# Optimization experiments

Measured on AMD Instinct MI355X. Metric: run time of the kernel, lower is better.

## Reference

```python
import jax, jax.numpy as jnp
import numpy as np

# Static configuration matching init_kwargs
LR_SHAPES = ((64, 64), (128, 128), (256, 256))
H0, W0 = LR_SHAPES[0]          # selected layer (layer_number = 0)
UP = (8, 8)                     # upscale factors -> output_dim = 64
OUT_DIM = UP[0] * UP[1]
KERNEL = (3, 3)
PAD = (1, 1)
BATCH = 64
WEIGHTS_IN = 189                # 9 + 36 + 144


def _unfold(x, kernel, stride, pad):
    """torch.F.unfold equivalent for NCHW input with C==1.
    x: (N, 1, H, W) -> (N, kh*kw, L) with row-major spatial positions."""
    patches = jax.lax.conv_general_dilated_patches(
        x,
        filter_shape=kernel,
        window_strides=stride,
        padding=((pad[0], pad[0]), (pad[1], pad[1])),
        dimension_numbers=('NCHW', 'OIHW', 'NCHW'),
    )  # (N, kh*kw, H_out, W_out)
    n, k, h, w = patches.shape
    return patches.reshape(n, k, h * w)


def setup_inputs() -> dict:
    key = jax.random.key(0)
    k0, k1, k2, kw = jax.random.split(key, 4)
    x0 = jax.random.normal(k0, (BATCH, 1, 64, 64), dtype=jnp.float32)
    x1 = jax.random.normal(k1, (BATCH, 1, 128, 128), dtype=jnp.float32)
    x2 = jax.random.normal(k2, (BATCH, 1, 256, 256), dtype=jnp.float32)
    # original uses uniform(-stdv, stdv) with tiny stdv; small-scale normal keeps
    # the softmax non-degenerate while matching the magnitude regime
    weight = jax.random.normal(kw, (WEIGHTS_IN, OUT_DIM), dtype=jnp.float32) * 0.01
    return {"x0": x0, "x1": x1, "x2": x2, "weight": weight}


def reference(x0, x1, x2, weight):
    xs = (x0, x1, x2)
    cols = []
    for j, (hj, wj) in enumerate(LR_SHAPES):
        s = (hj // H0, wj // W0)                       # scale vs selected layer
        f = (KERNEL[0] * s[0], KERNEL[1] * s[1])       # scaled kernel
        p = (PAD[0] * s[0], PAD[1] * s[1])             # scaled padding
        cols.append(_unfold(xs[j], f, s, p))           # (N, 9*s0*s1, L)
    X = jnp.concatenate(cols, axis=1)                  # (N, 189, L), L = H0*W0

    # per-pixel attention weights: matmul + ReLU + softmax
    logits = jax.nn.relu(jnp.einsum('nkl,ko->nlo', X, weight))  # (N, L, 64)
    soft = jax.nn.softmax(logits, axis=-1)                       # (N, L, 64)

    # reassemble: each LR pixel value scaled by its 64 attention weights (C==1)
    xsel = x0.reshape(x0.shape[0], H0 * W0)            # (N, L)
    out = xsel[:, :, None] * soft                      # (N, L, 64)

    # fold(kernel=1) == reshape to (N, 64, H0, W0)
    n = out.shape[0]
    out = out.transpose(0, 2, 1).reshape(n, OUT_DIM, H0, W0)

    # pixel shuffle -> (N, 1, H0*up0, W0*up1)
    out = out.reshape(n, 1, UP[0], UP[1], H0, W0)
    out = out.transpose(0, 1, 4, 2, 5, 3)
    return out.reshape(n, 1, H0 * UP[0], W0 * UP[1])
```

## Files before the change

kernel.cpp:

```cpp
#include <hip/hip_runtime.h>

typedef _Float16 f16;
typedef f16 f16x8 __attribute__((ext_vector_type(8)));
typedef f16 f16x4 __attribute__((ext_vector_type(4)));
typedef float f32x4 __attribute__((ext_vector_type(4)));

#define X0OFF 0
#define X1OFF 140
#define X2OFF 524
#define WSL   2048
#define LOG2E 1.4426950408889634f

__global__ void prep_wt(const float* __restrict__ W, f16* __restrict__ Wt) {
  const int f = blockIdx.x * 256 + threadIdx.x;
  const int s = f >> 8;
  const int t = (f >> 6) & 3;
  const int lane = f & 63;
  const int quad = lane >> 4, ln = lane & 15;
  const int n = t * 16 + ln;
  f16 vals[8];
  #pragma unroll
  for (int j = 0; j < 8; ++j) {
    int kp = s * 32 + quad * 8 + j;
    int orig = -1;
    if (kp < 16)      { int ki = kp >> 2, kj = kp & 3;                   if (ki < 3 && kj < 3) orig = 3*ki + kj; }
    else if (kp < 64) { int kk = kp - 16; int ki = kk >> 3, kj = kk & 7;  if (kj < 6)          orig = 9 + 6*ki + kj; }
    else              { int kk = kp - 64; int ki = kk >> 4, kj = kk & 15; if (kj < 12)         orig = 45 + 12*ki + kj; }
    vals[j] = (f16)((orig >= 0) ? W[orig * 64 + n] : 0.f);
  }
  *(f16x8*)(Wt + (size_t)f * 8) = *(const f16x8*)vals;
}

__global__ __launch_bounds__(256, 6) void fuse_kernel(
    const float* __restrict__ x0, const float* __restrict__ x1,
    const float* __restrict__ x2, const f16* __restrict__ Wt,
    float* __restrict__ out)
{
  __shared__ __align__(16) f16 tiles[4 * WSL];

  const int tid  = threadIdx.x;
  const int bid  = ((blockIdx.x & 7) << 8) | (blockIdx.x >> 3);
  const int nb   = bid >> 5;
  const int ty8  = (bid >> 2) & 7;
  const int tx   = bid & 3;
  const int lane = tid & 63;
  const int wid  = tid >> 6;
  const int ln   = lane & 15;
  const int quad = lane >> 4;

  f16* sl = tiles + wid * WSL;
  const f16* __restrict__ wfrag = Wt + (size_t)lane * 8;

  f32x4 v2[6];
  {
    const float* img = x2 + nb * 65536;
    #pragma unroll
    for (int i = 0; i < 6; ++i) {
      int idx = lane + 64 * i;
      int rr = idx / 22, c4 = idx - rr * 22;
      int gy = ty8 * 32 - 4 + 8 * wid + rr;
      int gx = tx * 64 - 8 + 4 * c4;
      bool inb = (i < 5 || lane < 32) && ((unsigned)gy < 256u) && ((unsigned)gx < 256u);
      v2[i] = inb ? *(const f32x4*)(img + gy * 256 + gx) : (f32x4){0.f, 0.f, 0.f, 0.f};
    }
  }

  {
    const float* img = x1 + nb * 16384;
    #pragma unroll
    for (int i = 0; i < 2; ++i) {
      int idx = lane + 64 * i;
      int rr = idx / 11, c4 = idx - rr * 11;
      int gy = ty8 * 16 - 2 + 4 * wid + rr;
      int gx = tx * 32 - 4 + 4 * c4;
      bool ok  = (i < 1 || lane < 24);
      bool inb = ok && ((unsigned)gy < 128u) && ((unsigned)gx < 128u);
      f32x4 t = inb ? *(const f32x4*)(img + gy * 128 + gx) : (f32x4){0.f, 0.f, 0.f, 0.f};
      if (ok) {
        f16x4 h; h[0] = (f16)t[0]; h[1] = (f16)t[1]; h[2] = (f16)t[2]; h[3] = (f16)t[3];
        *(f16x4*)&sl[X1OFF + rr * 48 + 4 * c4] = h;
      }
    }
  }
  {
    const float* img = x0 + nb * 4096;
    int rr = lane / 6, c4 = lane - rr * 6;
    int gy = ty8 * 8 - 1 + 2 * wid + rr;
    int gx = tx * 16 - 4 + 4 * c4;
    bool ok  = lane < 30;
    bool inb = ok && ((unsigned)gy < 64u) && ((unsigned)gx < 64u);
    f32x4 t = inb ? *(const f32x4*)(img + gy * 64 + gx) : (f32x4){0.f, 0.f, 0.f, 0.f};
    if (ok) {
      f16x4 h; h[0] = (f16)t[0]; h[1] = (f16)t[1]; h[2] = (f16)t[2]; h[3] = (f16)t[3];
      *(f16x4*)&sl[X0OFF + rr * 28 + 4 * c4] = h;
    }
  }

  float xs[2];
  #pragma unroll
  for (int cc = 0; cc < 2; ++cc)
    xs[cc] = x0[nb * 4096 + (ty8 * 8 + 2 * wid + cc) * 64 + tx * 16 + ln];

  #pragma unroll
  for (int i = 0; i < 6; ++i) {
    if (i < 5 || lane < 32) {
      int idx = lane + 64 * i;
      int rr = idx / 22, c4 = idx - rr * 22;
      f16x4 h; h[0] = (f16)v2[i][0]; h[1] = (f16)v2[i][1];
      h[2] = (f16)v2[i][2]; h[3] = (f16)v2[i][3];
      *(f16x4*)&sl[X2OFF + rr * 92 + 4 * c4] = h;
    }
  }

  f16x8 bf0[4];
  #pragma unroll
  for (int t = 0; t < 4; ++t)
    bf0[t] = *(const f16x8*)(wfrag + t * 512);


  f32x4 acc[2][4];
  #pragma unroll
  for (int c = 0; c < 2; ++c)
    #pragma unroll
    for (int t = 0; t < 4; ++t)
      acc[c][t] = (f32x4){0.f, 0.f, 0.f, 0.f};

  {
    #pragma unroll
    for (int cc = 0; cc < 2; ++cc) {
      f16x8 a;
      if (quad < 2) {
        const int a0 = X0OFF + (cc + 2 * quad) * 28 + ln + 3;
        #pragma unroll
        for (int j = 0; j < 4; ++j) a[j]     = sl[a0 + j];
        #pragma unroll
        for (int j = 0; j < 4; ++j) a[4 + j] = sl[a0 + 28 + j];
      } else {
        const int a1 = X1OFF + (2 * cc + quad - 2) * 48 + 2 * ln + 2;
        #pragma unroll
        for (int j = 0; j < 8; ++j) a[j] = sl[a1 + j];
      }
      #pragma unroll
      for (int t = 0; t < 4; ++t)
        acc[cc][t] = __builtin_amdgcn_mfma_f32_16x16x32_f16(bf0[t], a, acc[cc][t], 0, 0, 0);
    }
  }
  {
    f16x8 bf[4];
    #pragma unroll
    for (int t = 0; t < 4; ++t)
      bf[t] = *(const f16x8*)(wfrag + (4 + t) * 512);
    #pragma unroll
    for (int cc = 0; cc < 2; ++cc) {
      const int a1 = X1OFF + (2 * cc + 2 + quad) * 48 + 2 * ln + 2;
      f16x8 a;
      #pragma unroll
      for (int j = 0; j < 8; ++j) a[j] = sl[a1 + j];
      #pragma unroll
      for (int t = 0; t < 4; ++t)
        acc[cc][t] = __builtin_amdgcn_mfma_f32_16x16x32_f16(bf[t], a, acc[cc][t], 0, 0, 0);
    }
  }
  #pragma unroll 3
  for (int s = 2; s < 8; ++s) {
    f16x8 bf[4];
    #pragma unroll
    for (int t = 0; t < 4; ++t)
      bf[t] = *(const f16x8*)(wfrag + (s * 4 + t) * 512);
    #pragma unroll
    for (int cc = 0; cc < 2; ++cc) {
      const int b2 = X2OFF + (4 * cc + 2 * (s - 2) + (quad >> 1)) * 92 + 4 * ln + 4 + 8 * (quad & 1);
      f16x4 lo = *(const f16x4*)&sl[b2];
      f16x4 hi = *(const f16x4*)&sl[b2 + 4];
      f16x8 a;
      a[0] = lo[0]; a[1] = lo[1]; a[2] = lo[2]; a[3] = lo[3];
      a[4] = hi[0]; a[5] = hi[1]; a[6] = hi[2]; a[7] = hi[3];
      #pragma unroll
      for (int t = 0; t < 4; ++t)
        acc[cc][t] = __builtin_amdgcn_mfma_f32_16x16x32_f16(bf[t], a, acc[cc][t], 0, 0, 0);
    }
  }

  const int gx8 = (tx * 16 + ln) * 8;
  #pragma unroll
  for (int cc = 0; cc < 2; ++cc) {
    float v[4][4];
    float m = 0.f;
    #pragma unroll
    for (int t = 0; t < 4; ++t)
      #pragma unroll
      for (int r = 0; r < 4; ++r) {
        float x = fmaxf(acc[cc][t][r], 0.f);
        v[t][r] = x;
        m = fmaxf(m, x);
      }
    m = fmaxf(m, __shfl_xor(m, 16));
    m = fmaxf(m, __shfl_xor(m, 32));

    float sden = 0.f;
    #pragma unroll
    for (int t = 0; t < 4; ++t)
      #pragma unroll
      for (int r = 0; r < 4; ++r) {
        float e = exp2f((v[t][r] - m) * LOG2E);
        v[t][r] = e;
        sden += e;
      }
    sden += __shfl_xor(sden, 16);
    sden += __shfl_xor(sden, 32);

    const float sc = xs[cc] * __builtin_amdgcn_rcpf(sden);
    const int gy = ty8 * 8 + 2 * wid + cc;
    float* op = out + nb * 262144 + (gy * 8 + (quad >> 1)) * 512 + gx8 + 4 * (quad & 1);
    #pragma unroll
    for (int t = 0; t < 4; ++t) {
      f32x4 w;
      w[0] = v[t][0] * sc; w[1] = v[t][1] * sc;
      w[2] = v[t][2] * sc; w[3] = v[t][3] * sc;
      *(f32x4*)(op + t * 1024) = w;
    }
  }
}

extern "C" void kernel_launch(void* const* d_in, const int* in_sizes, int n_in,
                              void* d_out, int out_size, void* d_ws, size_t ws_size,
                              hipStream_t stream) {
  const float* x0 = (const float*)d_in[0];
  const float* x1 = (const float*)d_in[1];
  const float* x2 = (const float*)d_in[2];
  const float* W  = (const float*)d_in[3];
  float* outp     = (float*)d_out;
  f16* Wt         = (f16*)d_ws;

  prep_wt<<<dim3(8), dim3(256), 0, stream>>>(W, Wt);
  fuse_kernel<<<dim3(2048), dim3(256), 0, stream>>>(x0, x1, x2, Wt, outp);
}
```

Measured before the change: 108.8 us.

## Load x2 MFMA fragments directly from global memory instead of staging in LDS

The x2 patch tile is no longer staged through shared memory. Each lane reads its f32x4 fragments straight from global memory, using clamped addresses and masks for padding, and converts them to f16 in registers just before the MFMAs. This removes the LDS writes and reads for the largest input and shrinks the per-wave LDS slice from 2048 to 544 halves, with the x2 stage now issued ahead of the x0/x1 stages. The cost is redundant global loads across lanes that depend on cache hits, more address arithmetic, and a lower occupancy hint in launch_bounds (5 instead of 6).

```diff
diff --git a/kernel.cpp b/kernel.cpp
--- a/kernel.cpp
+++ b/kernel.cpp
@@ -7,8 +7,7 @@
 
 #define X0OFF 0
 #define X1OFF 140
-#define X2OFF 524
-#define WSL   2048
+#define WSL   544
 #define LOG2E 1.4426950408889634f
 
 __global__ void prep_wt(const float* __restrict__ W, f16* __restrict__ Wt) {
@@ -31,7 +30,7 @@
   *(f16x8*)(Wt + (size_t)f * 8) = *(const f16x8*)vals;
 }
 
-__global__ __launch_bounds__(256, 6) void fuse_kernel(
+__global__ __launch_bounds__(256, 5) void fuse_kernel(
     const float* __restrict__ x0, const float* __restrict__ x1,
     const float* __restrict__ x2, const f16* __restrict__ Wt,
     float* __restrict__ out)
@@ -50,36 +49,30 @@
 
   f16* sl = tiles + wid * WSL;
   const f16* __restrict__ wfrag = Wt + (size_t)lane * 8;
-
-  f32x4 v2[6];
-  {
-    const float* img = x2 + nb * 65536;
-    #pragma unroll
-    for (int i = 0; i < 6; ++i) {
-      int idx = lane + 64 * i;
-      int rr = idx / 22, c4 = idx - rr * 22;
-      int gy = ty8 * 32 - 4 + 8 * wid + rr;
-      int gx = tx * 64 - 8 + 4 * c4;
-      bool inb = (i < 5 || lane < 32) && ((unsigned)gy < 256u) && ((unsigned)gx < 256u);
-      v2[i] = inb ? *(const f32x4*)(img + gy * 256 + gx) : (f32x4){0.f, 0.f, 0.f, 0.f};
-    }
-  }
-
+  const float* __restrict__ img2 = x2 + nb * 65536;
+
+  f32x4 v1a, v1b, v0;
+  int w1a_off, w1b_off, w0_off;
+  bool ok1b, ok0;
   {
     const float* img = x1 + nb * 16384;
-    #pragma unroll
-    for (int i = 0; i < 2; ++i) {
-      int idx = lane + 64 * i;
+    {
+      int rr = lane / 11, c4 = lane - rr * 11;
+      int gy = ty8 * 16 - 2 + 4 * wid + rr;
+      int gx = tx * 32 - 4 + 4 * c4;
+      bool inb = ((unsigned)gy < 128u) && ((unsigned)gx < 128u);
+      v1a = inb ? *(const f32x4*)(img + gy * 128 + gx) : (f32x4){0.f, 0.f, 0.f, 0.f};
+      w1a_off = X1OFF + rr * 48 + 4 * c4;
+    }
+    {
+      int idx = lane + 64;
       int rr = idx / 11, c4 = idx - rr * 11;
       int gy = ty8 * 16 - 2 + 4 * wid + rr;
       int gx = tx * 32 - 4 + 4 * c4;
-      bool ok  = (i < 1 || lane < 24);
-      bool inb = ok && ((unsigned)gy < 128u) && ((unsigned)gx < 128u);
-      f32x4 t = inb ? *(const f32x4*)(img + gy * 128 + gx) : (f32x4){0.f, 0.f, 0.f, 0.f};
-      if (ok) {
-        f16x4 h; h[0] = (f16)t[0]; h[1] = (f16)t[1]; h[2] = (f16)t[2]; h[3] = (f16)t[3];
-        *(f16x4*)&sl[X1OFF + rr * 48 + 4 * c4] = h;
-      }
+      ok1b = lane < 24;
+      bool inb = ok1b && ((unsigned)gy < 128u) && ((unsigned)gx < 128u);
+      v1b = inb ? *(const f32x4*)(img + gy * 128 + gx) : (f32x4){0.f, 0.f, 0.f, 0.f};
+      w1b_off = X1OFF + rr * 48 + 4 * c4;
     }
   }
   {
@@ -87,13 +80,10 @@
     int rr = lane / 6, c4 = lane - rr * 6;
     int gy = ty8 * 8 - 1 + 2 * wid + rr;
     int gx = tx * 16 - 4 + 4 * c4;
-    bool ok  = lane < 30;
-    bool inb = ok && ((unsigned)gy < 64u) && ((unsigned)gx < 64u);
-    f32x4 t = inb ? *(const f32x4*)(img + gy * 64 + gx) : (f32x4){0.f, 0.f, 0.f, 0.f};
-    if (ok) {
-      f16x4 h; h[0] = (f16)t[0]; h[1] = (f16)t[1]; h[2] = (f16)t[2]; h[3] = (f16)t[3];
-      *(f16x4*)&sl[X0OFF + rr * 28 + 4 * c4] = h;
-    }
+    ok0 = lane < 30;
+    bool inb = ok0 && ((unsigned)gy < 64u) && ((unsigned)gx < 64u);
+    v0 = inb ? *(const f32x4*)(img + gy * 64 + gx) : (f32x4){0.f, 0.f, 0.f, 0.f};
+    w0_off = X0OFF + rr * 28 + 4 * c4;
   }
 
   float xs[2];
@@ -101,22 +91,41 @@
   for (int cc = 0; cc < 2; ++cc)
     xs[cc] = x0[nb * 4096 + (ty8 * 8 + 2 * wid + cc) * 64 + tx * 16 + ln];
 
-  #pragma unroll
-  for (int i = 0; i < 6; ++i) {
-    if (i < 5 || lane < 32) {
-      int idx = lane + 64 * i;
-      int rr = idx / 22, c4 = idx - rr * 22;
-      f16x4 h; h[0] = (f16)v2[i][0]; h[1] = (f16)v2[i][1];
-      h[2] = (f16)v2[i][2]; h[3] = (f16)v2[i][3];
-      *(f16x4*)&sl[X2OFF + rr * 92 + 4 * c4] = h;
-    }
-  }
-
-  f16x8 bf0[4];
+  const int  gxlo   = tx * 64 - 8 + 4 * ln + 4 + 8 * (quad & 1);
+  const bool oklo   = (unsigned)gxlo <= 252u;
+  const bool okhi   = (unsigned)(gxlo + 4) <= 252u;
+  const int  gxlo_c = gxlo < 0 ? 0 : (gxlo > 252 ? 252 : gxlo);
+  const int  gxhi_c = (gxlo + 4) < 0 ? 0 : ((gxlo + 4) > 252 ? 252 : (gxlo + 4));
+  const int  gy0    = ty8 * 32 - 4 + 8 * wid + (quad >> 1);
+
+  f32x4 lo2[2], hi2[2];
+  bool  gyok2[2];
+  #pragma unroll
+  for (int cc = 0; cc < 2; ++cc) {
+    int gy  = gy0 + 4 * cc;
+    gyok2[cc] = (unsigned)gy < 256u;
+    int gyc = gy < 0 ? 0 : (gy > 255 ? 255 : gy);
+    const float* prow = img2 + gyc * 256;
+    lo2[cc] = *(const f32x4*)(prow + gxlo_c);
+    hi2[cc] = *(const f32x4*)(prow + gxhi_c);
+  }
+  f16x8 bf2[4];
   #pragma unroll
   for (int t = 0; t < 4; ++t)
-    bf0[t] = *(const f16x8*)(wfrag + t * 512);
-
+    bf2[t] = *(const f16x8*)(wfrag + (8 + t) * 512);
+
+  {
+    f16x4 h; h[0] = (f16)v1a[0]; h[1] = (f16)v1a[1]; h[2] = (f16)v1a[2]; h[3] = (f16)v1a[3];
+    *(f16x4*)&sl[w1a_off] = h;
+  }
+  if (ok1b) {
+    f16x4 h; h[0] = (f16)v1b[0]; h[1] = (f16)v1b[1]; h[2] = (f16)v1b[2]; h[3] = (f16)v1b[3];
+    *(f16x4*)&sl[w1b_off] = h;
+  }
+  if (ok0) {
+    f16x4 h; h[0] = (f16)v0[0]; h[1] = (f16)v0[1]; h[2] = (f16)v0[2]; h[3] = (f16)v0[3];
+    *(f16x4*)&sl[w0_off] = h;
+  }
 
   f32x4 acc[2][4];
   #pragma unroll
@@ -125,7 +134,48 @@
     for (int t = 0; t < 4; ++t)
       acc[c][t] = (f32x4){0.f, 0.f, 0.f, 0.f};
 
-  {
+  #pragma unroll
+  for (int cc = 0; cc < 2; ++cc) {
+    f32x4 lo = (gyok2[cc] && oklo) ? lo2[cc] : (f32x4){0.f, 0.f, 0.f, 0.f};
+    f32x4 hi = (gyok2[cc] && okhi) ? hi2[cc] : (f32x4){0.f, 0.f, 0.f, 0.f};
+    f16x8 a;
+    #pragma unroll
+    for (int j = 0; j < 4; ++j) { a[j] = (f16)lo[j]; a[4 + j] = (f16)hi[j]; }
+    #pragma unroll
+    for (int t = 0; t < 4; ++t)
+      acc[cc][t] = __builtin_amdgcn_mfma_f32_16x16x32_f16(bf2[t], a, acc[cc][t], 0, 0, 0);
+  }
+
+  #pragma unroll
+  for (int s = 3; s < 8; ++s) {
+    f16x8 bf[4];
+    #pragma unroll
+    for (int t = 0; t < 4; ++t)
+      bf[t] = *(const f16x8*)(wfrag + (s * 4 + t) * 512);
+    #pragma unroll
+    for (int cc = 0; cc < 2; ++cc) {
+      int gy  = gy0 + 4 * cc + 2 * (s - 2);
+      bool gyok = (unsigned)gy < 256u;
+      int gyc = gy < 0 ? 0 : (gy > 255 ? 255 : gy);
+      const float* prow = img2 + gyc * 256;
+      f32x4 lo = *(const f32x4*)(prow + gxlo_c);
+      f32x4 hi = *(const f32x4*)(prow + gxhi_c);
+      lo = (gyok && oklo) ? lo : (f32x4){0.f, 0.f, 0.f, 0.f};
+      hi = (gyok && okhi) ? hi : (f32x4){0.f, 0.f, 0.f, 0.f};
+      f16x8 a;
+      #pragma unroll
+      for (int j = 0; j < 4; ++j) { a[j] = (f16)lo[j]; a[4 + j] = (f16)hi[j]; }
+      #pragma unroll
+      for (int t = 0; t < 4; ++t)
+        acc[cc][t] = __builtin_amdgcn_mfma_f32_16x16x32_f16(bf[t], a, acc[cc][t], 0, 0, 0);
+    }
+  }
+
+  {
+    f16x8 bf[4];
+    #pragma unroll
+    for (int t = 0; t < 4; ++t)
+      bf[t] = *(const f16x8*)(wfrag + t * 512);
     #pragma unroll
     for (int cc = 0; cc < 2; ++cc) {
       f16x8 a;
@@ -142,7 +192,7 @@
       }
       #pragma unroll
       for (int t = 0; t < 4; ++t)
-        acc[cc][t] = __builtin_amdgcn_mfma_f32_16x16x32_f16(bf0[t], a, acc[cc][t], 0, 0, 0);
+        acc[cc][t] = __builtin_amdgcn_mfma_f32_16x16x32_f16(bf[t], a, acc[cc][t], 0, 0, 0);
     }
   }
   {
@@ -156,25 +206,6 @@
       f16x8 a;
       #pragma unroll
       for (int j = 0; j < 8; ++j) a[j] = sl[a1 + j];
-      #pragma unroll
-      for (int t = 0; t < 4; ++t)
-        acc[cc][t] = __builtin_amdgcn_mfma_f32_16x16x32_f16(bf[t], a, acc[cc][t], 0, 0, 0);
-    }
-  }
-  #pragma unroll 3
-  for (int s = 2; s < 8; ++s) {
-    f16x8 bf[4];
-    #pragma unroll
-    for (int t = 0; t < 4; ++t)
-      bf[t] = *(const f16x8*)(wfrag + (s * 4 + t) * 512);
-    #pragma unroll
-    for (int cc = 0; cc < 2; ++cc) {
-      const int b2 = X2OFF + (4 * cc + 2 * (s - 2) + (quad >> 1)) * 92 + 4 * ln + 4 + 8 * (quad & 1);
-      f16x4 lo = *(const f16x4*)&sl[b2];
-      f16x4 hi = *(const f16x4*)&sl[b2 + 4];
-      f16x8 a;
-      a[0] = lo[0]; a[1] = lo[1]; a[2] = lo[2]; a[3] = lo[3];
-      a[4] = hi[0]; a[5] = hi[1]; a[6] = hi[2]; a[7] = hi[3];
       #pragma unroll
       for (int t = 0; t < 4; ++t)
         acc[cc][t] = __builtin_amdgcn_mfma_f32_16x16x32_f16(bf[t], a, acc[cc][t], 0, 0, 0);
```

Result: slower. 121.5 us (+11.7%).
